# Kernel tuning notes

Measured on AMD Instinct MI355X. Metric: run time of the kernel, lower is better.

## Reference

```python
import jax, jax.numpy as jnp
from jax import lax
import numpy as np

B, T, CIN, COUT = 64, 16384, 8, 8
N_A, N_B = 3, 3


def setup_inputs() -> dict:
    key = jax.random.key(0)
    k1, k2, k3, k4 = jax.random.split(key, 4)
    u = jax.random.normal(k1, (B, T, CIN), dtype=jnp.float32)
    x0 = jax.random.normal(k2, (B, N_A, COUT), dtype=jnp.float32)
    # Small AR coefficients so the IIR recursion is stable (sum |a_k| < 1).
    a_coeff = jax.random.uniform(k3, (N_A, COUT), dtype=jnp.float32,
                                 minval=-0.15, maxval=0.15)
    b_coeff = jax.random.normal(k4, (N_B + 1, CIN, COUT), dtype=jnp.float32)
    return {"u": u, "x0": x0, "a_coeff": a_coeff, "b_coeff": b_coeff}


def reference(u, x0, a_coeff, b_coeff):
    n_b = b_coeff.shape[0] - 1
    n_a = a_coeff.shape[0]
    # Causal FIR part: pad front of time axis, valid conv, channels_last.
    u_pad = jnp.pad(u, ((0, 0), (n_b, 0), (0, 0)))
    b_u = lax.conv_general_dilated(
        u_pad, b_coeff, window_strides=(1,), padding='VALID',
        dimension_numbers=('NWC', 'WIO', 'NWC'))  # [B, T, COUT]
    if n_a == 0:
        return b_u
    # Fold initial condition x0 into the first time step.
    first = b_u[:, 0, :] + jnp.einsum('to,bto->bo', jnp.flip(a_coeff, axis=0), x0)
    b_u = jnp.concatenate([first[:, None, :], b_u[:, 1:, :]], axis=1)
    # Stack n_a shifted copies (prepend tail of x0): [B, n_a, T, COUT]
    stacked = jnp.stack(
        [jnp.concatenate([x0[:, n_a - idx:, :], b_u[:, idx:, :]], axis=1)
         for idx in range(n_a)], axis=1)
    # Companion-style transition: a_ss[s, n, o] = a_coeff[n, o] if n >= s else 0.
    a_ss = jnp.stack(
        [jnp.pad(a_coeff[idx:, :], ((idx, 0), (0, 0))) for idx in range(n_a)],
        axis=0)  # [n_a, n_a, COUT]

    def a_apply(x, y):
        return jnp.einsum('sno,bnto->bsto', a_ss, x) + y

    y = lax.associative_scan(a_apply, stacked, axis=2)
    return y[:, 0, :, :]  # [B, T, COUT]
```

## Files before the change

### kernel.cpp

```cpp
#include <hip/hip_runtime.h>

#define T_SZ   16384
#define CIN    8
#define COUT   8
#define NPART  16
#define PART_T 1024
#define NCHUNK 32
#define CHT    32
#define GRID_BLOCKS (64 * NPART)
#define BAR_OFFSET_BYTES (1 << 17)

struct V3 { float x, y, z; };
__device__ __forceinline__ V3 mkv3(float a, float b, float c) { V3 r; r.x=a; r.y=b; r.z=c; return r; }
__device__ __forceinline__ V3 vadd3(V3 a, V3 b) { return mkv3(a.x+b.x, a.y+b.y, a.z+b.z); }
__device__ __forceinline__ V3 vfma3(V3 acc, float s, V3 w) {
  return mkv3(fmaf(s, w.x, acc.x), fmaf(s, w.y, acc.y), fmaf(s, w.z, acc.z));
}
__device__ __forceinline__ V3 aappf(float a0, float a1, float a2, V3 v) {
  float t2 = a2 * v.z;
  float t1 = fmaf(a1, v.y, t2);
  return mkv3(fmaf(a0, v.x, t1), t1, t2);
}
__device__ __forceinline__ V3 comb(float a0, float a1, float a2, V3 l, V3 r) {
  return vadd3(aappf(a0, a1, a2, l), r);
}

struct Row { float4 lo, hi; };
__device__ __forceinline__ Row ldrow(const float* p) {
  Row r; r.lo = *(const float4*)p; r.hi = *(const float4*)(p + 4); return r;
}
__device__ __forceinline__ Row zrow() { Row r; r.lo = make_float4(0.f,0.f,0.f,0.f); r.hi = r.lo; return r; }
__device__ __forceinline__ float rdot(const Row& r, const float* w) {
  float s = r.lo.x * w[0];
  s = fmaf(r.lo.y, w[1], s); s = fmaf(r.lo.z, w[2], s); s = fmaf(r.lo.w, w[3], s);
  s = fmaf(r.hi.x, w[4], s); s = fmaf(r.hi.y, w[5], s); s = fmaf(r.hi.z, w[6], s);
  s = fmaf(r.hi.w, w[7], s);
  return s;
}

struct Pre {
  float bv[CHT];
  V3 e0, e1, E5;
  float a0, a1, a2;
  int o, c, p, b, t0;
};

__device__ __forceinline__ void preamble(
    Pre& P, const float* __restrict__ u, const float* __restrict__ x0,
    const float* __restrict__ ac, const float* __restrict__ bc)
{
  const int j = threadIdx.x;
  P.o = j & 7;  P.c = j >> 3;
  P.p = blockIdx.x & 15;  P.b = blockIdx.x >> 4;
  const int o = P.o;
  P.a0 = ac[0*COUT + o];  P.a1 = ac[1*COUT + o];  P.a2 = ac[2*COUT + o];
  const float a0 = P.a0, a1 = P.a1, a2 = P.a2;

  float w0[8], w1[8], w2[8], w3[8];
#pragma unroll
  for (int i = 0; i < 8; ++i) {
    w0[i] = bc[(0*CIN + i)*COUT + o];
    w1[i] = bc[(1*CIN + i)*COUT + o];
    w2[i] = bc[(2*CIN + i)*COUT + o];
    w3[i] = bc[(3*CIN + i)*COUT + o];
  }

  const float* ub = u + (size_t)P.b * T_SZ * CIN;
  P.t0 = P.p * PART_T + P.c * CHT;
  const int t0 = P.t0;

  {
    Row ra, rb, rc;
    if (t0 == 0) { ra = zrow(); rb = zrow(); rc = zrow(); }
    else {
      ra = ldrow(ub + (size_t)(t0 - 3) * CIN);
      rb = ldrow(ub + (size_t)(t0 - 2) * CIN);
      rc = ldrow(ub + (size_t)(t0 - 1) * CIN);
    }
#pragma unroll
    for (int r = 0; r < CHT; ++r) {
      Row rd = ldrow(ub + (size_t)(t0 + r) * CIN);
      P.bv[r] = rdot(ra, w0) + rdot(rb, w1) + rdot(rc, w2) + rdot(rd, w3);
      ra = rb; rb = rc; rc = rd;
    }
  }

  P.e0 = mkv3(0,0,0);  P.e1 = mkv3(0,0,0);
  if (t0 == 0) {
    float x00 = x0[((size_t)P.b*3 + 0)*COUT + o];
    float x01 = x0[((size_t)P.b*3 + 1)*COUT + o];
    float x02 = x0[((size_t)P.b*3 + 2)*COUT + o];
    float first = P.bv[0] + a2*x00 + a1*x01 + a0*x02;
    P.e0 = mkv3(first, x02, x01);
    P.e1 = mkv3(P.bv[1], P.bv[1], x02);
  }

  V3 gt[6];
  gt[0] = mkv3(1.f,1.f,1.f);
#pragma unroll
  for (int k = 1; k <= 5; ++k) gt[k] = aappf(a0,a1,a2, gt[k-1]);
  V3 acc;
  if (t0 == 0) {
    V3 q0 = P.e0, q1 = P.e1;
#pragma unroll
    for (int k = 0; k < 5; ++k) q0 = aappf(a0,a1,a2, q0);
#pragma unroll
    for (int k = 0; k < 4; ++k) q1 = aappf(a0,a1,a2, q1);
    acc = vadd3(q0, q1);
#pragma unroll
    for (int r = 2; r < CHT; ++r) acc = vfma3(acc, P.bv[r], gt[5 - __popc(r)]);
  } else {
    acc = mkv3(0,0,0);
#pragma unroll
    for (int r = 0; r < CHT; ++r) acc = vfma3(acc, P.bv[r], gt[5 - __popc(r)]);
  }
  P.E5 = acc;
}

__global__ __launch_bounds__(256) void ldtf_p1(
    const float* __restrict__ u, const float* __restrict__ x0,
    const float* __restrict__ ac, const float* __restrict__ bc,
    float* __restrict__ ws)
{
  __shared__ V3 s_E5[NCHUNK*8];
  __shared__ V3 s_tr[30*8];

  Pre P;
  preamble(P, u, x0, ac, bc);
  const int j = threadIdx.x, o = P.o;
  const float a0 = P.a0, a1 = P.a1, a2 = P.a2;

  s_E5[P.c*8 + o] = P.E5;
  __syncthreads();
  if (j < 128) { int i = j >> 3; s_tr[i*8+o]      = comb(a0,a1,a2, s_E5[(2*i)*8+o],    s_E5[(2*i+1)*8+o]); }
  __syncthreads();
  if (j < 64)  { int i = j >> 3; s_tr[(16+i)*8+o] = comb(a0,a1,a2, s_tr[(2*i)*8+o],    s_tr[(2*i+1)*8+o]); }
  __syncthreads();
  if (j < 32)  { int i = j >> 3; s_tr[(24+i)*8+o] = comb(a0,a1,a2, s_tr[(16+2*i)*8+o], s_tr[(16+2*i+1)*8+o]); }
  __syncthreads();
  if (j < 16)  { int i = j >> 3; s_tr[(28+i)*8+o] = comb(a0,a1,a2, s_tr[(24+2*i)*8+o], s_tr[(24+2*i+1)*8+o]); }
  __syncthreads();
  if (j < 8) {
    V3 rt = comb(a0,a1,a2, s_tr[28*8+o], s_tr[29*8+o]);
    float* wp = ws + ((size_t)(P.b*NPART + P.p)*8 + o)*3;
    wp[0] = rt.x; wp[1] = rt.y; wp[2] = rt.z;
  }
}

#define POOL_FLOATS 8448

__global__ __launch_bounds__(256) void ldtf_p2(
    const float* __restrict__ u, const float* __restrict__ x0,
    const float* __restrict__ ac, const float* __restrict__ bc,
    float* __restrict__ out, const float* __restrict__ ws)
{
  __shared__ __align__(16) float s_pool[POOL_FLOATS];
  V3* s_E5 = (V3*)s_pool;
  V3* s_tr = (V3*)s_pool + 256;
  V3* s_mt = (V3*)s_pool + 496;
  float* s_out = s_pool;

  Pre P;
  preamble(P, u, x0, ac, bc);
  const int j = threadIdx.x, o = P.o, c = P.c, p = P.p, b = P.b;
  const float a0 = P.a0, a1 = P.a1, a2 = P.a2;

  s_E5[c*8 + o] = P.E5;
  if (j < 128) {
    int c2 = j >> 3;
    const float* wp = ws + ((size_t)(b*NPART + c2)*8 + o)*3;
    s_mt[c2*8+o] = mkv3(wp[0], wp[1], wp[2]);
  }
  __syncthreads();

  if (j < 128) { int i = j >> 3; s_tr[i*8+o]      = comb(a0,a1,a2, s_E5[(2*i)*8+o],    s_E5[(2*i+1)*8+o]); }
  else         { int i = (j-128) >> 3; if (i < 8) s_mt[(16+i)*8+o] = comb(a0,a1,a2, s_mt[(2*i)*8+o], s_mt[(2*i+1)*8+o]); }
  __syncthreads();
  if (j < 64)  { int i = j >> 3; s_tr[(16+i)*8+o] = comb(a0,a1,a2, s_tr[(2*i)*8+o],    s_tr[(2*i+1)*8+o]); }
  else if (j >= 128) { int i = (j-128) >> 3; if (i < 4) s_mt[(24+i)*8+o] = comb(a0,a1,a2, s_mt[(16+2*i)*8+o], s_mt[(16+2*i+1)*8+o]); }
  __syncthreads();
  if (j < 32)  { int i = j >> 3; s_tr[(24+i)*8+o] = comb(a0,a1,a2, s_tr[(16+2*i)*8+o], s_tr[(16+2*i+1)*8+o]); }
  else if (j >= 128) { int i = (j-128) >> 3; if (i < 2) s_mt[(28+i)*8+o] = comb(a0,a1,a2, s_mt[(24+2*i)*8+o], s_mt[(24+2*i+1)*8+o]); }
  __syncthreads();
  if (j < 16)  { int i = j >> 3; s_tr[(28+i)*8+o] = comb(a0,a1,a2, s_tr[(24+2*i)*8+o], s_tr[(24+2*i+1)*8+o]); }
  __syncthreads();

  V3 sig = mkv3(0,0,0);
  if ((p >> 3) & 1) sig = comb(a0,a1,a2, sig, s_mt[(28 + (p>>3) - 1)*8 + o]);
  if ((p >> 2) & 1) sig = comb(a0,a1,a2, sig, s_mt[(24 + (p>>2) - 1)*8 + o]);
  if ((p >> 1) & 1) sig = comb(a0,a1,a2, sig, s_mt[(16 + (p>>1) - 1)*8 + o]);
  if (p & 1)        sig = comb(a0,a1,a2, sig, s_mt[(p - 1)*8 + o]);
  if ((c >> 4) & 1) sig = comb(a0,a1,a2, sig, s_tr[(28 + (c>>4) - 1)*8 + o]);
  if ((c >> 3) & 1) sig = comb(a0,a1,a2, sig, s_tr[(24 + (c>>3) - 1)*8 + o]);
  if ((c >> 2) & 1) sig = comb(a0,a1,a2, sig, s_tr[(16 + (c>>2) - 1)*8 + o]);
  if ((c >> 1) & 1) sig = comb(a0,a1,a2, sig, s_tr[((c>>1) - 1)*8 + o]);
  if (c & 1)        sig = comb(a0,a1,a2, sig, s_E5[(c - 1)*8 + o]);

  V3 tau;
  {
    int q = p + 1;
    if (q == 16) tau = comb(a0,a1,a2, s_mt[28*8+o], s_mt[29*8+o]);
    else {
      tau = mkv3(0,0,0);
      if ((q >> 3) & 1) tau = comb(a0,a1,a2, tau, s_mt[(28 + (q>>3) - 1)*8 + o]);
      if ((q >> 2) & 1) tau = comb(a0,a1,a2, tau, s_mt[(24 + (q>>2) - 1)*8 + o]);
      if ((q >> 1) & 1) tau = comb(a0,a1,a2, tau, s_mt[(16 + (q>>1) - 1)*8 + o]);
      if (q & 1)        tau = comb(a0,a1,a2, tau, s_mt[(q - 1)*8 + o]);
    }
  }
  __syncthreads();

  if (c >= 1) s_out[(c - 1)*264 + 31*8 + o] = sig.x;
  if (c == NCHUNK - 1) s_out[31*264 + 31*8 + o] = tau.x;

  {
    V3 st[5];
#pragma unroll
    for (int r = 0; r < CHT - 1; ++r) {
      V3 v = mkv3(P.bv[r], P.bv[r], P.bv[r]);
      if (P.t0 == 0) { if (r == 0) v = P.e0; if (r == 1) v = P.e1; }
      if (r & 1)          v = comb(a0,a1,a2, st[0], v);
      if ((r & 3) == 3)   v = comb(a0,a1,a2, st[1], v);
      if ((r & 7) == 7)   v = comb(a0,a1,a2, st[2], v);
      if ((r & 15) == 15) v = comb(a0,a1,a2, st[3], v);
      const int lvl = (r & 1) ? (((r & 3) == 3) ? (((r & 7) == 7) ? (((r & 15) == 15) ? 4 : 3) : 2) : 1) : 0;
      st[lvl] = v;
      const int i = r + 1;
      V3 acc = sig;
      if (i & 16) acc = comb(a0,a1,a2, acc, st[4]);
      if (i & 8)  acc = comb(a0,a1,a2, acc, st[3]);
      if (i & 4)  acc = comb(a0,a1,a2, acc, st[2]);
      if (i & 2)  acc = comb(a0,a1,a2, acc, st[1]);
      if (i & 1)  acc = comb(a0,a1,a2, acc, st[0]);
      s_out[c*264 + r*8 + o] = acc.x;
    }
  }
  __syncthreads();

  float* og = out + ((size_t)b * T_SZ + (size_t)p * PART_T) * COUT;
#pragma unroll
  for (int it = 0; it < 8; ++it) {
    int f = (it * 256 + j) * 4;
    float4 v = *(const float4*)&s_out[(f >> 8) * 264 + (f & 255)];
    *(float4*)&og[f] = v;
  }
}

__global__ __launch_bounds__(256) void ldtf_fused(
    const float* __restrict__ u, const float* __restrict__ x0,
    const float* __restrict__ ac, const float* __restrict__ bc,
    float* __restrict__ out, float* __restrict__ ws,
    unsigned int* __restrict__ bar)
{
  __shared__ __align__(16) float s_pool[POOL_FLOATS];
  V3* s_E5 = (V3*)s_pool;
  V3* s_tr = (V3*)s_pool + 256;
  V3* s_mt = (V3*)s_pool + 496;
  float* s_out = s_pool;

  Pre P;
  preamble(P, u, x0, ac, bc);
  const int j = threadIdx.x, o = P.o, c = P.c, p = P.p, b = P.b;
  const float a0 = P.a0, a1 = P.a1, a2 = P.a2;

  s_E5[c*8 + o] = P.E5;
  __syncthreads();
  if (j < 128) { int i = j >> 3; s_tr[i*8+o]      = comb(a0,a1,a2, s_E5[(2*i)*8+o],    s_E5[(2*i+1)*8+o]); }
  __syncthreads();
  if (j < 64)  { int i = j >> 3; s_tr[(16+i)*8+o] = comb(a0,a1,a2, s_tr[(2*i)*8+o],    s_tr[(2*i+1)*8+o]); }
  __syncthreads();
  if (j < 32)  { int i = j >> 3; s_tr[(24+i)*8+o] = comb(a0,a1,a2, s_tr[(16+2*i)*8+o], s_tr[(16+2*i+1)*8+o]); }
  __syncthreads();
  if (j < 16)  { int i = j >> 3; s_tr[(28+i)*8+o] = comb(a0,a1,a2, s_tr[(24+2*i)*8+o], s_tr[(24+2*i+1)*8+o]); }
  __syncthreads();
  if (j < 8) {
    V3 rt = comb(a0,a1,a2, s_tr[28*8+o], s_tr[29*8+o]);
    float* wp = ws + ((size_t)(b*NPART + p)*8 + o)*3;
    wp[0] = rt.x; wp[1] = rt.y; wp[2] = rt.z;
  }
  __syncthreads();
  if (j == 0) {
    __threadfence();
    atomicAdd(bar, 1u);
    while (__hip_atomic_load(bar, __ATOMIC_ACQUIRE, __HIP_MEMORY_SCOPE_AGENT)
           < (unsigned)GRID_BLOCKS) {
      __builtin_amdgcn_s_sleep(2);
    }
  }
  __syncthreads();
  __threadfence();

  if (j < 128) {
    int c2 = j >> 3;
    const float* wp = ws + ((size_t)(b*NPART + c2)*8 + o)*3;
    s_mt[c2*8+o] = mkv3(wp[0], wp[1], wp[2]);
  }
  __syncthreads();
  if (j < 64) { int i = j >> 3; s_mt[(16+i)*8+o] = comb(a0,a1,a2, s_mt[(2*i)*8+o],    s_mt[(2*i+1)*8+o]); }
  __syncthreads();
  if (j < 32) { int i = j >> 3; s_mt[(24+i)*8+o] = comb(a0,a1,a2, s_mt[(16+2*i)*8+o], s_mt[(16+2*i+1)*8+o]); }
  __syncthreads();
  if (j < 16) { int i = j >> 3; s_mt[(28+i)*8+o] = comb(a0,a1,a2, s_mt[(24+2*i)*8+o], s_mt[(24+2*i+1)*8+o]); }
  __syncthreads();

  V3 sig = mkv3(0,0,0);
  if ((p >> 3) & 1) sig = comb(a0,a1,a2, sig, s_mt[(28 + (p>>3) - 1)*8 + o]);
  if ((p >> 2) & 1) sig = comb(a0,a1,a2, sig, s_mt[(24 + (p>>2) - 1)*8 + o]);
  if ((p >> 1) & 1) sig = comb(a0,a1,a2, sig, s_mt[(16 + (p>>1) - 1)*8 + o]);
  if (p & 1)        sig = comb(a0,a1,a2, sig, s_mt[(p - 1)*8 + o]);
  if ((c >> 4) & 1) sig = comb(a0,a1,a2, sig, s_tr[(28 + (c>>4) - 1)*8 + o]);
  if ((c >> 3) & 1) sig = comb(a0,a1,a2, sig, s_tr[(24 + (c>>3) - 1)*8 + o]);
  if ((c >> 2) & 1) sig = comb(a0,a1,a2, sig, s_tr[(16 + (c>>2) - 1)*8 + o]);
  if ((c >> 1) & 1) sig = comb(a0,a1,a2, sig, s_tr[((c>>1) - 1)*8 + o]);
  if (c & 1)        sig = comb(a0,a1,a2, sig, s_E5[(c - 1)*8 + o]);

  V3 tau;
  {
    int q = p + 1;
    if (q == 16) tau = comb(a0,a1,a2, s_mt[28*8+o], s_mt[29*8+o]);
    else {
      tau = mkv3(0,0,0);
      if ((q >> 3) & 1) tau = comb(a0,a1,a2, tau, s_mt[(28 + (q>>3) - 1)*8 + o]);
      if ((q >> 2) & 1) tau = comb(a0,a1,a2, tau, s_mt[(24 + (q>>2) - 1)*8 + o]);
      if ((q >> 1) & 1) tau = comb(a0,a1,a2, tau, s_mt[(16 + (q>>1) - 1)*8 + o]);
      if (q & 1)        tau = comb(a0,a1,a2, tau, s_mt[(q - 1)*8 + o]);
    }
  }
  __syncthreads();

  if (c >= 1) s_out[(c - 1)*264 + 31*8 + o] = sig.x;
  if (c == NCHUNK - 1) s_out[31*264 + 31*8 + o] = tau.x;

  {
    V3 st[5];
#pragma unroll
    for (int r = 0; r < CHT - 1; ++r) {
      V3 v = mkv3(P.bv[r], P.bv[r], P.bv[r]);
      if (P.t0 == 0) { if (r == 0) v = P.e0; if (r == 1) v = P.e1; }
      if (r & 1)          v = comb(a0,a1,a2, st[0], v);
      if ((r & 3) == 3)   v = comb(a0,a1,a2, st[1], v);
      if ((r & 7) == 7)   v = comb(a0,a1,a2, st[2], v);
      if ((r & 15) == 15) v = comb(a0,a1,a2, st[3], v);
      const int lvl = (r & 1) ? (((r & 3) == 3) ? (((r & 7) == 7) ? (((r & 15) == 15) ? 4 : 3) : 2) : 1) : 0;
      st[lvl] = v;
      const int i = r + 1;
      V3 acc = sig;
      if (i & 16) acc = comb(a0,a1,a2, acc, st[4]);
      if (i & 8)  acc = comb(a0,a1,a2, acc, st[3]);
      if (i & 4)  acc = comb(a0,a1,a2, acc, st[2]);
      if (i & 2)  acc = comb(a0,a1,a2, acc, st[1]);
      if (i & 1)  acc = comb(a0,a1,a2, acc, st[0]);
      s_out[c*264 + r*8 + o] = acc.x;
    }
  }
  __syncthreads();

  float* og = out + ((size_t)b * T_SZ + (size_t)p * PART_T) * COUT;
#pragma unroll
  for (int it = 0; it < 8; ++it) {
    int f = (it * 256 + j) * 4;
    float4 v = *(const float4*)&s_out[(f >> 8) * 264 + (f & 255)];
    *(float4*)&og[f] = v;
  }
}

extern "C" void kernel_launch(void* const* d_in, const int* in_sizes, int n_in,
                              void* d_out, int out_size, void* d_ws, size_t ws_size,
                              hipStream_t stream) {
  const float* u  = (const float*)d_in[0];
  const float* x0 = (const float*)d_in[1];
  const float* ac = (const float*)d_in[2];
  const float* bc = (const float*)d_in[3];
  float* outp = (float*)d_out;
  float* wsp  = (float*)d_ws;
  (void)in_sizes; (void)n_in; (void)out_size;

  static int fused_ok = -1;
  if (fused_ok < 0) {
    int nb = 0, ncu = 0, dev = 0;
    hipGetDevice(&dev);
    hipDeviceProp_t prop;
    if (hipGetDeviceProperties(&prop, dev) == hipSuccess) ncu = prop.multiProcessorCount;
    if (hipOccupancyMaxActiveBlocksPerMultiprocessor(&nb, ldtf_fused, 256, 0) != hipSuccess) nb = 0;
    fused_ok = (nb > 0 && ncu > 0 && (long)nb * ncu >= GRID_BLOCKS &&
                ws_size >= (size_t)BAR_OFFSET_BYTES + 16) ? 1 : 0;
  }

  if (fused_ok == 1) {
    unsigned int* bar = (unsigned int*)((char*)d_ws + BAR_OFFSET_BYTES);
    hipMemsetAsync(bar, 0, sizeof(unsigned int), stream);
    ldtf_fused<<<dim3(GRID_BLOCKS), dim3(256), 0, stream>>>(u, x0, ac, bc, outp, wsp, bar);
  } else {
    ldtf_p1<<<dim3(GRID_BLOCKS), dim3(256), 0, stream>>>(u, x0, ac, bc, wsp);
    ldtf_p2<<<dim3(GRID_BLOCKS), dim3(256), 0, stream>>>(u, x0, ac, bc, outp, wsp);
  }
}
```

Baseline: 131.5 us.

## Halve grid to 512 blocks with 64-step chunks staged in shared memory

The fused persistent kernel now uses 8 partitions of 2048 timesteps per batch instead of 16 of 1024, so there are 512 blocks and each thread scans 64 steps. The FIR outputs are computed once into a shared-memory buffer and reused for the scan, instead of being held in registers from a preamble. Results are written back in place to that buffer before the coalesced store. Fewer blocks should make the grid barrier cheaper and shrink the cross-partition tree, at the cost of longer serial per-thread work, more shared memory per block, and lower occupancy (launch bounds of 2 blocks).

```diff
diff --git a/kernel.cpp b/kernel.cpp
--- a/kernel.cpp
+++ b/kernel.cpp
@@ -7,8 +7,14 @@
 #define PART_T 1024
 #define NCHUNK 32
 #define CHT    32
-#define GRID_BLOCKS (64 * NPART)
 #define BAR_OFFSET_BYTES (1 << 17)
+
+#define NPART2  8
+#define PART2_T 2048
+#define NCHK2   32
+#define CHT2    64
+#define BVS     516
+#define GRID2   (64 * NPART2)
 
 struct V3 { float x, y, z; };
 __device__ __forceinline__ V3 mkv3(float a, float b, float c) { V3 r; r.x=a; r.y=b; r.z=c; return r; }
@@ -246,26 +252,82 @@
   }
 }
 
-__global__ __launch_bounds__(256) void ldtf_fused(
+__global__ __launch_bounds__(256, 2) void ldtf_fused512(
     const float* __restrict__ u, const float* __restrict__ x0,
     const float* __restrict__ ac, const float* __restrict__ bc,
     float* __restrict__ out, float* __restrict__ ws,
     unsigned int* __restrict__ bar)
 {
-  __shared__ __align__(16) float s_pool[POOL_FLOATS];
-  V3* s_E5 = (V3*)s_pool;
-  V3* s_tr = (V3*)s_pool + 256;
-  V3* s_mt = (V3*)s_pool + 496;
-  float* s_out = s_pool;
-
-  Pre P;
-  preamble(P, u, x0, ac, bc);
-  const int j = threadIdx.x, o = P.o, c = P.c, p = P.p, b = P.b;
-  const float a0 = P.a0, a1 = P.a1, a2 = P.a2;
-
-  s_E5[c*8 + o] = P.E5;
-  __syncthreads();
-  if (j < 128) { int i = j >> 3; s_tr[i*8+o]      = comb(a0,a1,a2, s_E5[(2*i)*8+o],    s_E5[(2*i+1)*8+o]); }
+  __shared__ __align__(16) float s_bv[NCHK2 * BVS];
+  __shared__ V3 s_lf[NCHK2 * 8];
+  __shared__ V3 s_tr[30 * 8];
+  __shared__ V3 s_mt[15 * 8];
+
+  const int j = threadIdx.x;
+  const int o = j & 7, c = j >> 3;
+  const int p = blockIdx.x & 7, b = blockIdx.x >> 3;
+
+  const float a0 = ac[0*COUT + o], a1 = ac[1*COUT + o], a2 = ac[2*COUT + o];
+
+  float w0[8], w1[8], w2[8], w3[8];
+#pragma unroll
+  for (int i = 0; i < 8; ++i) {
+    w0[i] = bc[(0*CIN + i)*COUT + o];
+    w1[i] = bc[(1*CIN + i)*COUT + o];
+    w2[i] = bc[(2*CIN + i)*COUT + o];
+    w3[i] = bc[(3*CIN + i)*COUT + o];
+  }
+
+  const float* ub = u + (size_t)b * T_SZ * CIN;
+  const int t0 = p * PART2_T + c * CHT2;
+  const bool z0 = (t0 == 0);
+
+  V3 gt[7];
+  gt[0] = mkv3(1.f,1.f,1.f);
+#pragma unroll
+  for (int k = 1; k <= 6; ++k) gt[k] = aappf(a0,a1,a2, gt[k-1]);
+
+  float bv0r = 0.f, bv1r = 0.f;
+  V3 accE = mkv3(0,0,0);
+  float* bvp = &s_bv[c * BVS + o];
+  {
+    Row ra, rb, rc;
+    if (z0) { ra = zrow(); rb = zrow(); rc = zrow(); }
+    else {
+      ra = ldrow(ub + (size_t)(t0 - 3) * CIN);
+      rb = ldrow(ub + (size_t)(t0 - 2) * CIN);
+      rc = ldrow(ub + (size_t)(t0 - 1) * CIN);
+    }
+#pragma unroll
+    for (int r = 0; r < CHT2; ++r) {
+      Row rd = ldrow(ub + (size_t)(t0 + r) * CIN);
+      float bvr = rdot(ra, w0) + rdot(rb, w1) + rdot(rc, w2) + rdot(rd, w3);
+      bvp[r*8] = bvr;
+      if (r == 0) bv0r = bvr;
+      if (r == 1) bv1r = bvr;
+      if (!(z0 && r < 2)) accE = vfma3(accE, bvr, gt[6 - __popc(r)]);
+      ra = rb; rb = rc; rc = rd;
+    }
+  }
+  V3 e0 = mkv3(0,0,0), e1 = mkv3(0,0,0);
+  if (z0) {
+    float x00 = x0[((size_t)b*3 + 0)*COUT + o];
+    float x01 = x0[((size_t)b*3 + 1)*COUT + o];
+    float x02 = x0[((size_t)b*3 + 2)*COUT + o];
+    float first = bv0r + a2*x00 + a1*x01 + a0*x02;
+    e0 = mkv3(first, x02, x01);
+    e1 = mkv3(bv1r, bv1r, x02);
+    V3 q0 = e0, q1 = e1;
+#pragma unroll
+    for (int k = 0; k < 6; ++k) q0 = aappf(a0,a1,a2, q0);
+#pragma unroll
+    for (int k = 0; k < 5; ++k) q1 = aappf(a0,a1,a2, q1);
+    accE = vadd3(accE, vadd3(q0, q1));
+  }
+  s_lf[c*8 + o] = accE;
+  __syncthreads();
+
+  if (j < 128) { int i = j >> 3; s_tr[i*8+o]      = comb(a0,a1,a2, s_lf[(2*i)*8+o],    s_lf[(2*i+1)*8+o]); }
   __syncthreads();
   if (j < 64)  { int i = j >> 3; s_tr[(16+i)*8+o] = comb(a0,a1,a2, s_tr[(2*i)*8+o],    s_tr[(2*i+1)*8+o]); }
   __syncthreads();
@@ -275,91 +337,96 @@
   __syncthreads();
   if (j < 8) {
     V3 rt = comb(a0,a1,a2, s_tr[28*8+o], s_tr[29*8+o]);
-    float* wp = ws + ((size_t)(b*NPART + p)*8 + o)*3;
-    wp[0] = rt.x; wp[1] = rt.y; wp[2] = rt.z;
-  }
+    float* wp = ws + ((size_t)(b*NPART2 + p)*8 + o)*3;
+    __hip_atomic_store(wp + 0, rt.x, __ATOMIC_RELAXED, __HIP_MEMORY_SCOPE_AGENT);
+    __hip_atomic_store(wp + 1, rt.y, __ATOMIC_RELAXED, __HIP_MEMORY_SCOPE_AGENT);
+    __hip_atomic_store(wp + 2, rt.z, __ATOMIC_RELAXED, __HIP_MEMORY_SCOPE_AGENT);
+  }
+
   __syncthreads();
   if (j == 0) {
     __threadfence();
     atomicAdd(bar, 1u);
     while (__hip_atomic_load(bar, __ATOMIC_ACQUIRE, __HIP_MEMORY_SCOPE_AGENT)
-           < (unsigned)GRID_BLOCKS) {
+           < (unsigned)GRID2) {
       __builtin_amdgcn_s_sleep(2);
     }
   }
   __syncthreads();
   __threadfence();
 
-  if (j < 128) {
-    int c2 = j >> 3;
-    const float* wp = ws + ((size_t)(b*NPART + c2)*8 + o)*3;
-    s_mt[c2*8+o] = mkv3(wp[0], wp[1], wp[2]);
-  }
-  __syncthreads();
-  if (j < 64) { int i = j >> 3; s_mt[(16+i)*8+o] = comb(a0,a1,a2, s_mt[(2*i)*8+o],    s_mt[(2*i+1)*8+o]); }
-  __syncthreads();
-  if (j < 32) { int i = j >> 3; s_mt[(24+i)*8+o] = comb(a0,a1,a2, s_mt[(16+2*i)*8+o], s_mt[(16+2*i+1)*8+o]); }
-  __syncthreads();
-  if (j < 16) { int i = j >> 3; s_mt[(28+i)*8+o] = comb(a0,a1,a2, s_mt[(24+2*i)*8+o], s_mt[(24+2*i+1)*8+o]); }
+  if (j < 64) {
+    int pp = j >> 3;
+    const float* wp = ws + ((size_t)(b*NPART2 + pp)*8 + o)*3;
+    float rx = __hip_atomic_load(wp + 0, __ATOMIC_RELAXED, __HIP_MEMORY_SCOPE_AGENT);
+    float ry = __hip_atomic_load(wp + 1, __ATOMIC_RELAXED, __HIP_MEMORY_SCOPE_AGENT);
+    float rz = __hip_atomic_load(wp + 2, __ATOMIC_RELAXED, __HIP_MEMORY_SCOPE_AGENT);
+    s_mt[pp*8 + o] = mkv3(rx, ry, rz);
+  }
+  __syncthreads();
+  if (j < 32) { int i = j >> 3; s_mt[(8+i)*8+o]  = comb(a0,a1,a2, s_mt[(2*i)*8+o],   s_mt[(2*i+1)*8+o]); }
+  __syncthreads();
+  if (j < 16) { int i = j >> 3; s_mt[(12+i)*8+o] = comb(a0,a1,a2, s_mt[(8+2*i)*8+o], s_mt[(8+2*i+1)*8+o]); }
+  __syncthreads();
+  if (j < 8)  {                 s_mt[14*8+o]     = comb(a0,a1,a2, s_mt[12*8+o],      s_mt[13*8+o]); }
   __syncthreads();
 
   V3 sig = mkv3(0,0,0);
-  if ((p >> 3) & 1) sig = comb(a0,a1,a2, sig, s_mt[(28 + (p>>3) - 1)*8 + o]);
-  if ((p >> 2) & 1) sig = comb(a0,a1,a2, sig, s_mt[(24 + (p>>2) - 1)*8 + o]);
-  if ((p >> 1) & 1) sig = comb(a0,a1,a2, sig, s_mt[(16 + (p>>1) - 1)*8 + o]);
+  if ((p >> 2) & 1) sig = comb(a0,a1,a2, sig, s_mt[(12 + (p>>2) - 1)*8 + o]);
+  if ((p >> 1) & 1) sig = comb(a0,a1,a2, sig, s_mt[(8  + (p>>1) - 1)*8 + o]);
   if (p & 1)        sig = comb(a0,a1,a2, sig, s_mt[(p - 1)*8 + o]);
   if ((c >> 4) & 1) sig = comb(a0,a1,a2, sig, s_tr[(28 + (c>>4) - 1)*8 + o]);
   if ((c >> 3) & 1) sig = comb(a0,a1,a2, sig, s_tr[(24 + (c>>3) - 1)*8 + o]);
   if ((c >> 2) & 1) sig = comb(a0,a1,a2, sig, s_tr[(16 + (c>>2) - 1)*8 + o]);
   if ((c >> 1) & 1) sig = comb(a0,a1,a2, sig, s_tr[((c>>1) - 1)*8 + o]);
-  if (c & 1)        sig = comb(a0,a1,a2, sig, s_E5[(c - 1)*8 + o]);
+  if (c & 1)        sig = comb(a0,a1,a2, sig, s_lf[(c - 1)*8 + o]);
 
   V3 tau;
   {
     int q = p + 1;
-    if (q == 16) tau = comb(a0,a1,a2, s_mt[28*8+o], s_mt[29*8+o]);
+    if (q == 8) tau = s_mt[14*8+o];
     else {
       tau = mkv3(0,0,0);
-      if ((q >> 3) & 1) tau = comb(a0,a1,a2, tau, s_mt[(28 + (q>>3) - 1)*8 + o]);
-      if ((q >> 2) & 1) tau = comb(a0,a1,a2, tau, s_mt[(24 + (q>>2) - 1)*8 + o]);
-      if ((q >> 1) & 1) tau = comb(a0,a1,a2, tau, s_mt[(16 + (q>>1) - 1)*8 + o]);
+      if ((q >> 2) & 1) tau = comb(a0,a1,a2, tau, s_mt[(12 + (q>>2) - 1)*8 + o]);
+      if ((q >> 1) & 1) tau = comb(a0,a1,a2, tau, s_mt[(8  + (q>>1) - 1)*8 + o]);
       if (q & 1)        tau = comb(a0,a1,a2, tau, s_mt[(q - 1)*8 + o]);
     }
   }
-  __syncthreads();
-
-  if (c >= 1) s_out[(c - 1)*264 + 31*8 + o] = sig.x;
-  if (c == NCHUNK - 1) s_out[31*264 + 31*8 + o] = tau.x;
-
-  {
-    V3 st[5];
-#pragma unroll
-    for (int r = 0; r < CHT - 1; ++r) {
-      V3 v = mkv3(P.bv[r], P.bv[r], P.bv[r]);
-      if (P.t0 == 0) { if (r == 0) v = P.e0; if (r == 1) v = P.e1; }
+
+  if (c >= 1) s_bv[(c - 1)*BVS + 63*8 + o] = sig.x;
+  if (c == NCHK2 - 1) s_bv[(NCHK2 - 1)*BVS + 63*8 + o] = tau.x;
+
+  {
+    V3 st[6];
+#pragma unroll
+    for (int r = 0; r < CHT2 - 1; ++r) {
+      float bvr = bvp[r*8];
+      V3 v = mkv3(bvr, bvr, bvr);
+      if (z0) { if (r == 0) v = e0; if (r == 1) v = e1; }
       if (r & 1)          v = comb(a0,a1,a2, st[0], v);
       if ((r & 3) == 3)   v = comb(a0,a1,a2, st[1], v);
       if ((r & 7) == 7)   v = comb(a0,a1,a2, st[2], v);
       if ((r & 15) == 15) v = comb(a0,a1,a2, st[3], v);
-      const int lvl = (r & 1) ? (((r & 3) == 3) ? (((r & 7) == 7) ? (((r & 15) == 15) ? 4 : 3) : 2) : 1) : 0;
-      st[lvl] = v;
+      if ((r & 31) == 31) v = comb(a0,a1,a2, st[4], v);
+      st[__popc(r ^ (r + 1)) - 1] = v;
       const int i = r + 1;
       V3 acc = sig;
+      if (i & 32) acc = comb(a0,a1,a2, acc, st[5]);
       if (i & 16) acc = comb(a0,a1,a2, acc, st[4]);
       if (i & 8)  acc = comb(a0,a1,a2, acc, st[3]);
       if (i & 4)  acc = comb(a0,a1,a2, acc, st[2]);
       if (i & 2)  acc = comb(a0,a1,a2, acc, st[1]);
       if (i & 1)  acc = comb(a0,a1,a2, acc, st[0]);
-      s_out[c*264 + r*8 + o] = acc.x;
-    }
-  }
-  __syncthreads();
-
-  float* og = out + ((size_t)b * T_SZ + (size_t)p * PART_T) * COUT;
-#pragma unroll
-  for (int it = 0; it < 8; ++it) {
+      bvp[r*8] = acc.x;
+    }
+  }
+  __syncthreads();
+
+  float* og = out + ((size_t)b * T_SZ + (size_t)p * PART2_T) * COUT;
+#pragma unroll
+  for (int it = 0; it < 16; ++it) {
     int f = (it * 256 + j) * 4;
-    float4 v = *(const float4*)&s_out[(f >> 8) * 264 + (f & 255)];
+    float4 v = *(const float4*)&s_bv[(f >> 9) * BVS + (f & 511)];
     *(float4*)&og[f] = v;
   }
 }
@@ -381,17 +448,17 @@
     hipGetDevice(&dev);
     hipDeviceProp_t prop;
     if (hipGetDeviceProperties(&prop, dev) == hipSuccess) ncu = prop.multiProcessorCount;
-    if (hipOccupancyMaxActiveBlocksPerMultiprocessor(&nb, ldtf_fused, 256, 0) != hipSuccess) nb = 0;
-    fused_ok = (nb > 0 && ncu > 0 && (long)nb * ncu >= GRID_BLOCKS &&
+    if (hipOccupancyMaxActiveBlocksPerMultiprocessor(&nb, ldtf_fused512, 256, 0) != hipSuccess) nb = 0;
+    fused_ok = (nb > 0 && ncu > 0 && (long)nb * ncu >= GRID2 &&
                 ws_size >= (size_t)BAR_OFFSET_BYTES + 16) ? 1 : 0;
   }
 
   if (fused_ok == 1) {
     unsigned int* bar = (unsigned int*)((char*)d_ws + BAR_OFFSET_BYTES);
     hipMemsetAsync(bar, 0, sizeof(unsigned int), stream);
-    ldtf_fused<<<dim3(GRID_BLOCKS), dim3(256), 0, stream>>>(u, x0, ac, bc, outp, wsp, bar);
+    ldtf_fused512<<<dim3(GRID2), dim3(256), 0, stream>>>(u, x0, ac, bc, outp, wsp, bar);
   } else {
-    ldtf_p1<<<dim3(GRID_BLOCKS), dim3(256), 0, stream>>>(u, x0, ac, bc, wsp);
-    ldtf_p2<<<dim3(GRID_BLOCKS), dim3(256), 0, stream>>>(u, x0, ac, bc, outp, wsp);
-  }
-}
+    ldtf_p1<<<dim3(64 * NPART), dim3(256), 0, stream>>>(u, x0, ac, bc, wsp);
+    ldtf_p2<<<dim3(64 * NPART), dim3(256), 0, stream>>>(u, x0, ac, bc, outp, wsp);
+  }
+}
```

Result: no change. 132.4 us (+0.7%).

## Inline preamble, shrink shared memory, write outputs directly, add launch bounds

Applied to the files above, without the earlier changes.

Renames the fused kernel and inlines the FIR preamble. The chunk-local aggregate is now computed as a dot product with powers of the transition, and the kernel carries a __launch_bounds__(256,4) occupancy hint. The large shared output staging buffer and its final barrier are dropped, and each thread writes its scan outputs straight to global memory as strided scalar stores. Workspace exchange uses relaxed atomic loads and stores. This lowers LDS use and register pressure so more blocks fit per CU for the grid-wide barrier, at the cost of uncoalesced stores (each thread writes its own 4-byte element at a 32-byte stride within a wave).

```diff
diff --git a/kernel.cpp b/kernel.cpp
--- a/kernel.cpp
+++ b/kernel.cpp
@@ -246,26 +246,86 @@
   }
 }
 
-__global__ __launch_bounds__(256) void ldtf_fused(
+__global__ __launch_bounds__(256, 4) void ldtf_fused1024(
     const float* __restrict__ u, const float* __restrict__ x0,
     const float* __restrict__ ac, const float* __restrict__ bc,
     float* __restrict__ out, float* __restrict__ ws,
     unsigned int* __restrict__ bar)
 {
-  __shared__ __align__(16) float s_pool[POOL_FLOATS];
-  V3* s_E5 = (V3*)s_pool;
-  V3* s_tr = (V3*)s_pool + 256;
-  V3* s_mt = (V3*)s_pool + 496;
-  float* s_out = s_pool;
-
-  Pre P;
-  preamble(P, u, x0, ac, bc);
-  const int j = threadIdx.x, o = P.o, c = P.c, p = P.p, b = P.b;
-  const float a0 = P.a0, a1 = P.a1, a2 = P.a2;
-
-  s_E5[c*8 + o] = P.E5;
-  __syncthreads();
-  if (j < 128) { int i = j >> 3; s_tr[i*8+o]      = comb(a0,a1,a2, s_E5[(2*i)*8+o],    s_E5[(2*i+1)*8+o]); }
+  __shared__ V3 s_lf[NCHUNK*8];
+  __shared__ V3 s_tr[30*8];
+  __shared__ V3 s_mt[30*8];
+
+  const int j = threadIdx.x;
+  const int o = j & 7, c = j >> 3;
+  const int p = blockIdx.x & 15, b = blockIdx.x >> 4;
+
+  const float a0 = ac[0*COUT + o], a1 = ac[1*COUT + o], a2 = ac[2*COUT + o];
+
+  const float* ub = u + (size_t)b * T_SZ * CIN;
+  const int t0 = p * PART_T + c * CHT;
+  const bool z0 = (t0 == 0);
+
+  float bv[CHT];
+  {
+    float w0[8], w1[8], w2[8], w3[8];
+#pragma unroll
+    for (int i = 0; i < 8; ++i) {
+      w0[i] = bc[(0*CIN + i)*COUT + o];
+      w1[i] = bc[(1*CIN + i)*COUT + o];
+      w2[i] = bc[(2*CIN + i)*COUT + o];
+      w3[i] = bc[(3*CIN + i)*COUT + o];
+    }
+    Row ra, rb, rc;
+    if (z0) { ra = zrow(); rb = zrow(); rc = zrow(); }
+    else {
+      ra = ldrow(ub + (size_t)(t0 - 3) * CIN);
+      rb = ldrow(ub + (size_t)(t0 - 2) * CIN);
+      rc = ldrow(ub + (size_t)(t0 - 1) * CIN);
+    }
+#pragma unroll
+    for (int r = 0; r < CHT; ++r) {
+      Row rd = ldrow(ub + (size_t)(t0 + r) * CIN);
+      bv[r] = rdot(ra, w0) + rdot(rb, w1) + rdot(rc, w2) + rdot(rd, w3);
+      ra = rb; rb = rc; rc = rd;
+    }
+  }
+
+  V3 e0 = mkv3(0,0,0), e1 = mkv3(0,0,0);
+  if (z0) {
+    float x00 = x0[((size_t)b*3 + 0)*COUT + o];
+    float x01 = x0[((size_t)b*3 + 1)*COUT + o];
+    float x02 = x0[((size_t)b*3 + 2)*COUT + o];
+    float first = bv[0] + a2*x00 + a1*x01 + a0*x02;
+    e0 = mkv3(first, x02, x01);
+    e1 = mkv3(bv[1], bv[1], x02);
+  }
+
+  {
+    V3 gt[6];
+    gt[0] = mkv3(1.f,1.f,1.f);
+#pragma unroll
+    for (int k = 1; k <= 5; ++k) gt[k] = aappf(a0,a1,a2, gt[k-1]);
+    V3 acc;
+    if (z0) {
+      V3 q0 = e0, q1 = e1;
+#pragma unroll
+      for (int k = 0; k < 5; ++k) q0 = aappf(a0,a1,a2, q0);
+#pragma unroll
+      for (int k = 0; k < 4; ++k) q1 = aappf(a0,a1,a2, q1);
+      acc = vadd3(q0, q1);
+#pragma unroll
+      for (int r = 2; r < CHT; ++r) acc = vfma3(acc, bv[r], gt[5 - __popc(r)]);
+    } else {
+      acc = mkv3(0,0,0);
+#pragma unroll
+      for (int r = 0; r < CHT; ++r) acc = vfma3(acc, bv[r], gt[5 - __popc(r)]);
+    }
+    s_lf[c*8 + o] = acc;
+  }
+  __syncthreads();
+
+  if (j < 128) { int i = j >> 3; s_tr[i*8+o]      = comb(a0,a1,a2, s_lf[(2*i)*8+o],    s_lf[(2*i+1)*8+o]); }
   __syncthreads();
   if (j < 64)  { int i = j >> 3; s_tr[(16+i)*8+o] = comb(a0,a1,a2, s_tr[(2*i)*8+o],    s_tr[(2*i+1)*8+o]); }
   __syncthreads();
@@ -276,8 +336,11 @@
   if (j < 8) {
     V3 rt = comb(a0,a1,a2, s_tr[28*8+o], s_tr[29*8+o]);
     float* wp = ws + ((size_t)(b*NPART + p)*8 + o)*3;
-    wp[0] = rt.x; wp[1] = rt.y; wp[2] = rt.z;
-  }
+    __hip_atomic_store(wp + 0, rt.x, __ATOMIC_RELAXED, __HIP_MEMORY_SCOPE_AGENT);
+    __hip_atomic_store(wp + 1, rt.y, __ATOMIC_RELAXED, __HIP_MEMORY_SCOPE_AGENT);
+    __hip_atomic_store(wp + 2, rt.z, __ATOMIC_RELAXED, __HIP_MEMORY_SCOPE_AGENT);
+  }
+
   __syncthreads();
   if (j == 0) {
     __threadfence();
@@ -293,7 +356,10 @@
   if (j < 128) {
     int c2 = j >> 3;
     const float* wp = ws + ((size_t)(b*NPART + c2)*8 + o)*3;
-    s_mt[c2*8+o] = mkv3(wp[0], wp[1], wp[2]);
+    float rx = __hip_atomic_load(wp + 0, __ATOMIC_RELAXED, __HIP_MEMORY_SCOPE_AGENT);
+    float ry = __hip_atomic_load(wp + 1, __ATOMIC_RELAXED, __HIP_MEMORY_SCOPE_AGENT);
+    float rz = __hip_atomic_load(wp + 2, __ATOMIC_RELAXED, __HIP_MEMORY_SCOPE_AGENT);
+    s_mt[c2*8 + o] = mkv3(rx, ry, rz);
   }
   __syncthreads();
   if (j < 64) { int i = j >> 3; s_mt[(16+i)*8+o] = comb(a0,a1,a2, s_mt[(2*i)*8+o],    s_mt[(2*i+1)*8+o]); }
@@ -312,10 +378,14 @@
   if ((c >> 3) & 1) sig = comb(a0,a1,a2, sig, s_tr[(24 + (c>>3) - 1)*8 + o]);
   if ((c >> 2) & 1) sig = comb(a0,a1,a2, sig, s_tr[(16 + (c>>2) - 1)*8 + o]);
   if ((c >> 1) & 1) sig = comb(a0,a1,a2, sig, s_tr[((c>>1) - 1)*8 + o]);
-  if (c & 1)        sig = comb(a0,a1,a2, sig, s_E5[(c - 1)*8 + o]);
-
-  V3 tau;
-  {
+  if (c & 1)        sig = comb(a0,a1,a2, sig, s_lf[(c - 1)*8 + o]);
+
+  float* og = out + ((size_t)b * T_SZ + (size_t)t0) * COUT + o;
+
+  if (c >= 1) *(og - 8) = sig.x;
+
+  if (c == NCHUNK - 1) {
+    V3 tau;
     int q = p + 1;
     if (q == 16) tau = comb(a0,a1,a2, s_mt[28*8+o], s_mt[29*8+o]);
     else {
@@ -325,18 +395,15 @@
       if ((q >> 1) & 1) tau = comb(a0,a1,a2, tau, s_mt[(16 + (q>>1) - 1)*8 + o]);
       if (q & 1)        tau = comb(a0,a1,a2, tau, s_mt[(q - 1)*8 + o]);
     }
-  }
-  __syncthreads();
-
-  if (c >= 1) s_out[(c - 1)*264 + 31*8 + o] = sig.x;
-  if (c == NCHUNK - 1) s_out[31*264 + 31*8 + o] = tau.x;
+    og[31*8] = tau.x;
+  }
 
   {
     V3 st[5];
 #pragma unroll
     for (int r = 0; r < CHT - 1; ++r) {
-      V3 v = mkv3(P.bv[r], P.bv[r], P.bv[r]);
-      if (P.t0 == 0) { if (r == 0) v = P.e0; if (r == 1) v = P.e1; }
+      V3 v = mkv3(bv[r], bv[r], bv[r]);
+      if (z0) { if (r == 0) v = e0; if (r == 1) v = e1; }
       if (r & 1)          v = comb(a0,a1,a2, st[0], v);
       if ((r & 3) == 3)   v = comb(a0,a1,a2, st[1], v);
       if ((r & 7) == 7)   v = comb(a0,a1,a2, st[2], v);
@@ -350,17 +417,8 @@
       if (i & 4)  acc = comb(a0,a1,a2, acc, st[2]);
       if (i & 2)  acc = comb(a0,a1,a2, acc, st[1]);
       if (i & 1)  acc = comb(a0,a1,a2, acc, st[0]);
-      s_out[c*264 + r*8 + o] = acc.x;
-    }
-  }
-  __syncthreads();
-
-  float* og = out + ((size_t)b * T_SZ + (size_t)p * PART_T) * COUT;
-#pragma unroll
-  for (int it = 0; it < 8; ++it) {
-    int f = (it * 256 + j) * 4;
-    float4 v = *(const float4*)&s_out[(f >> 8) * 264 + (f & 255)];
-    *(float4*)&og[f] = v;
+      og[r*8] = acc.x;
+    }
   }
 }
 
@@ -381,7 +439,7 @@
     hipGetDevice(&dev);
     hipDeviceProp_t prop;
     if (hipGetDeviceProperties(&prop, dev) == hipSuccess) ncu = prop.multiProcessorCount;
-    if (hipOccupancyMaxActiveBlocksPerMultiprocessor(&nb, ldtf_fused, 256, 0) != hipSuccess) nb = 0;
+    if (hipOccupancyMaxActiveBlocksPerMultiprocessor(&nb, ldtf_fused1024, 256, 0) != hipSuccess) nb = 0;
     fused_ok = (nb > 0 && ncu > 0 && (long)nb * ncu >= GRID_BLOCKS &&
                 ws_size >= (size_t)BAR_OFFSET_BYTES + 16) ? 1 : 0;
   }
@@ -389,7 +447,7 @@
   if (fused_ok == 1) {
     unsigned int* bar = (unsigned int*)((char*)d_ws + BAR_OFFSET_BYTES);
     hipMemsetAsync(bar, 0, sizeof(unsigned int), stream);
-    ldtf_fused<<<dim3(GRID_BLOCKS), dim3(256), 0, stream>>>(u, x0, ac, bc, outp, wsp, bar);
+    ldtf_fused1024<<<dim3(GRID_BLOCKS), dim3(256), 0, stream>>>(u, x0, ac, bc, outp, wsp, bar);
   } else {
     ldtf_p1<<<dim3(GRID_BLOCKS), dim3(256), 0, stream>>>(u, x0, ac, bc, wsp);
     ldtf_p2<<<dim3(GRID_BLOCKS), dim3(256), 0, stream>>>(u, x0, ac, bc, outp, wsp);
```

Result: no change. 133.9 us (+1.8%).
